# Optimization experiments

Measured on AMD Instinct MI355X. Metric: run time of the kernel, lower is better.

## Reference

```python
import jax, jax.numpy as jnp
import numpy as np

MARGIN = 0.3
NUM_CLASSES = 1000


def setup_inputs() -> dict:
    key = jax.random.key(0)
    k1, k2 = jax.random.split(key)
    B, D = 8192, 256
    inputs = jax.random.normal(k1, (B, D), dtype=jnp.float32)
    targets = jax.random.randint(k2, (B,), 0, NUM_CLASSES, dtype=jnp.int64)
    return {"inputs": inputs, "targets": targets}


def reference(inputs, targets):
    # Squared Euclidean pairwise distances: ||x_i||^2 + ||x_j||^2 - 2 x_i.x_j
    sq = jnp.sum(inputs * inputs, axis=1)                      # [B]
    dist = sq[:, None] + sq[None, :] - 2.0 * (inputs @ inputs.T)  # [B, B]

    # Hard mining: per-row max over positives (same label, incl. self),
    # min over negatives, exactly as the torch per-row masked max/min loop.
    pos_mask = targets[:, None] == targets[None, :]            # [B, B] bool
    neg_inf = jnp.float32(-jnp.inf)
    pos_inf = jnp.float32(jnp.inf)
    dist_ap = jnp.max(jnp.where(pos_mask, dist, neg_inf), axis=1)  # [B]
    dist_an = jnp.min(jnp.where(pos_mask, pos_inf, dist), axis=1)  # [B]

    # MarginRankingLoss(margin)(dist_an, dist_ap, y=1) = mean relu(ap - an + m)
    loss = jnp.mean(jax.nn.relu(dist_ap - dist_an + MARGIN))
    prec = jnp.mean((dist_an > dist_ap).astype(jnp.float32))
    return (loss, prec)
```

## Files before the change

kernel.cpp:

```cpp
#include <hip/hip_runtime.h>
#include <hip/hip_bf16.h>

#define B_N 8192
#define D_K 256
#define MARGIN 0.3f

typedef float f32x4 __attribute__((ext_vector_type(4)));
typedef short s16x8 __attribute__((ext_vector_type(8)));

__device__ __forceinline__ unsigned fkey(float f) {
    unsigned u = __float_as_uint(f);
    return (u & 0x80000000u) ? ~u : (u | 0x80000000u);
}
__device__ __forceinline__ float kval(unsigned k) {
    return (k & 0x80000000u) ? __uint_as_float(k ^ 0x80000000u)
                             : __uint_as_float(~k);
}

__device__ __forceinline__ void load_lds16(const unsigned short* g,
                                           unsigned short* l) {
    __builtin_amdgcn_global_load_lds(
        (const __attribute__((address_space(1))) unsigned int*)g,
        (__attribute__((address_space(3))) unsigned int*)l, 16, 0, 0);
}

__global__ __launch_bounds__(256) void prep_kernel(const float* __restrict__ X,
        float* __restrict__ sq, unsigned* __restrict__ apk,
        unsigned* __restrict__ ank, unsigned short* __restrict__ Xp,
        float* __restrict__ acc2) {
    int row  = (blockIdx.x << 2) + (threadIdx.x >> 6);
    int lane = threadIdx.x & 63;
    const float4 v = reinterpret_cast<const float4*>(X + (size_t)row * D_K)[lane];

    float xs[4] = {v.x, v.y, v.z, v.w};
    ushort4 hv;
    unsigned short* hp = &hv.x;
    float s = 0.f;
    #pragma unroll
    for (int i = 0; i < 4; ++i) {
        __hip_bfloat16 h = __float2bfloat16(xs[i]);
        hp[i] = *reinterpret_cast<unsigned short*>(&h);
        float hf = __bfloat162float(h);
        s = fmaf(hf, hf, s);
    }
    *reinterpret_cast<ushort4*>(Xp + (size_t)row * D_K + lane * 4) = hv;

    #pragma unroll
    for (int o = 32; o > 0; o >>= 1) s += __shfl_down(s, o, 64);
    if (lane == 0) {
        sq[row]  = s;
        apk[row] = 0u;
        ank[row] = 0xFFFFFFFFu;
    }
    if (blockIdx.x == 0 && threadIdx.x == 0) {
        acc2[0] = 0.f; acc2[1] = 0.f;
        reinterpret_cast<unsigned*>(acc2)[2] = 0u;
    }
}

#define BM 128
#define BN 128

__global__ __launch_bounds__(256, 4) void dist_kernel(
        const unsigned short* __restrict__ Xp,
        const int* __restrict__ tgt, const float* __restrict__ sq,
        unsigned* __restrict__ apk, unsigned* __restrict__ ank) {
    __shared__ unsigned short Atile[128 * 64];
    __shared__ unsigned short Btile[128 * 64];

    const int t    = threadIdx.x;
    const int lane = t & 63;
    const int wave = t >> 6;
    const int wrow = (wave >> 1) * 64;
    const int wcol = (wave & 1) * 64;
    const int fr   = lane & 15;
    const int quad = lane >> 4;
    const float INF = __int_as_float(0x7f800000);

    int tt = blockIdx.x;
    int bx = (int)((sqrtf(8.f * (float)tt + 1.f) - 1.f) * 0.5f);
    while ((bx + 1) * (bx + 2) / 2 <= tt) ++bx;
    while (bx * (bx + 1) / 2 > tt) --bx;
    int by = tt - bx * (bx + 1) / 2;
    const int bm = by * BM;
    const int bn = bx * BN;

    const unsigned short* ag[4];
    const unsigned short* bg[4];
    unsigned short* al[4];
    unsigned short* bl[4];
    #pragma unroll
    for (int j = 0; j < 4; ++j) {
        int g = wave * 64 + j * 256 + lane;
        int r = g >> 3, s0 = g & 7;
        int u = s0 ^ (r & 7);
        ag[j] = Xp + (size_t)(bm + r) * D_K + u * 8;
        bg[j] = Xp + (size_t)(bn + r) * D_K + u * 8;
        al[j] = Atile + g * 8;
        bl[j] = Btile + g * 8;
    }

    f32x4 acc[4][4];
    #pragma unroll
    for (int i = 0; i < 4; ++i)
        #pragma unroll
        for (int j = 0; j < 4; ++j) acc[i][j] = (f32x4){0.f, 0.f, 0.f, 0.f};

    #pragma unroll 1
    for (int win = 0; win < 4; ++win) {
        __syncthreads();
        const int wo = win * 64;
        #pragma unroll
        for (int j = 0; j < 4; ++j) {
            load_lds16(ag[j] + wo, al[j]);
            load_lds16(bg[j] + wo, bl[j]);
        }
        __syncthreads();

        s16x8 a[4][2], b[4][2];
        #pragma unroll
        for (int mi = 0; mi < 4; ++mi) {
            int rb = (wrow + mi * 16 + fr) * 64;
            #pragma unroll
            for (int h = 0; h < 2; ++h) {
                int s = (h * 4 + quad) ^ (fr & 7);
                a[mi][h] = *reinterpret_cast<const s16x8*>(&Atile[rb + s * 8]);
            }
        }
        #pragma unroll
        for (int ni = 0; ni < 4; ++ni) {
            int rb = (wcol + ni * 16 + fr) * 64;
            #pragma unroll
            for (int h = 0; h < 2; ++h) {
                int s = (h * 4 + quad) ^ (fr & 7);
                b[ni][h] = *reinterpret_cast<const s16x8*>(&Btile[rb + s * 8]);
            }
        }
        #pragma unroll
        for (int mi = 0; mi < 4; ++mi)
            #pragma unroll
            for (int ni = 0; ni < 4; ++ni) {
                acc[mi][ni] = __builtin_amdgcn_mfma_f32_16x16x32_bf16(
                    a[mi][0], b[ni][0], acc[mi][ni], 0, 0, 0);
                acc[mi][ni] = __builtin_amdgcn_mfma_f32_16x16x32_bf16(
                    a[mi][1], b[ni][1], acc[mi][ni], 0, 0, 0);
            }
    }

    int   ct[4]; float csq[4];
    #pragma unroll
    for (int ni = 0; ni < 4; ++ni) {
        int c = bn + wcol + ni * 16 + fr;
        ct[ni] = tgt[c]; csq[ni] = sq[c];
    }
    float cap[4], can[4];
    #pragma unroll
    for (int ni = 0; ni < 4; ++ni) { cap[ni] = -INF; can[ni] = INF; }

    #pragma unroll
    for (int mi = 0; mi < 4; ++mi) {
        #pragma unroll
        for (int reg = 0; reg < 4; ++reg) {
            int rl = wrow + mi * 16 + quad * 4 + reg;
            int rt = tgt[bm + rl]; float rsq = sq[bm + rl];
            float rap = -INF, ran = INF;
            #pragma unroll
            for (int ni = 0; ni < 4; ++ni) {
                float d = rsq + csq[ni] - 2.f * acc[mi][ni][reg];
                bool pos = (rt == ct[ni]);
                if (pos) { rap = fmaxf(rap, d); cap[ni] = fmaxf(cap[ni], d); }
                else     { ran = fminf(ran, d); can[ni] = fminf(can[ni], d); }
            }
            #pragma unroll
            for (int o = 1; o < 16; o <<= 1) {
                rap = fmaxf(rap, __shfl_xor(rap, o, 64));
                ran = fminf(ran, __shfl_xor(ran, o, 64));
            }
            if (fr == 0) {
                atomicMax(&apk[bm + rl], fkey(rap));
                atomicMin(&ank[bm + rl], fkey(ran));
            }
        }
    }
    #pragma unroll
    for (int ni = 0; ni < 4; ++ni) {
        #pragma unroll
        for (int o = 16; o < 64; o <<= 1) {
            cap[ni] = fmaxf(cap[ni], __shfl_xor(cap[ni], o, 64));
            can[ni] = fminf(can[ni], __shfl_xor(can[ni], o, 64));
        }
    }
    if (lane < 16) {
        #pragma unroll
        for (int ni = 0; ni < 4; ++ni) {
            int c = bn + wcol + ni * 16 + lane;
            atomicMax(&apk[c], fkey(cap[ni]));
            atomicMin(&ank[c], fkey(can[ni]));
        }
    }
}

__global__ __launch_bounds__(256) void final_kernel(const unsigned* __restrict__ apk,
        const unsigned* __restrict__ ank, float* __restrict__ acc2,
        float* __restrict__ out) {
    __shared__ float s_sum[4], s_cnt[4];
    int i = blockIdx.x * 256 + threadIdx.x;
    float ap = kval(apk[i]);
    float an = kval(ank[i]);
    float v  = ap - an + MARGIN;
    float sum = v > 0.f ? v : 0.f;
    float cnt = an > ap ? 1.f : 0.f;
    #pragma unroll
    for (int o = 32; o > 0; o >>= 1) {
        sum += __shfl_down(sum, o, 64);
        cnt += __shfl_down(cnt, o, 64);
    }
    int wave = threadIdx.x >> 6, lane = threadIdx.x & 63;
    if (lane == 0) { s_sum[wave] = sum; s_cnt[wave] = cnt; }
    __syncthreads();
    if (threadIdx.x == 0) {
        float ts = 0.f, tc = 0.f;
        #pragma unroll
        for (int w = 0; w < 4; ++w) { ts += s_sum[w]; tc += s_cnt[w]; }
        atomicAdd(&acc2[0], ts);
        atomicAdd(&acc2[1], tc);
        __threadfence();
        unsigned ticket = atomicAdd(reinterpret_cast<unsigned*>(acc2) + 2, 1u);
        if (ticket == gridDim.x - 1) {
            float fs = atomicAdd(&acc2[0], 0.f);
            float fc = atomicAdd(&acc2[1], 0.f);
            out[0] = fs / (float)B_N;
            out[1] = fc / (float)B_N;
        }
    }
}

extern "C" void kernel_launch(void* const* d_in, const int* in_sizes, int n_in,
                              void* d_out, int out_size, void* d_ws, size_t ws_size,
                              hipStream_t stream) {
    const float* X   = (const float*)d_in[0];
    const int*   tgt = (const int*)d_in[1];

    char* ws = (char*)d_ws;
    float*          sq   = (float*)ws;
    unsigned*       apk  = (unsigned*)(ws + 32768);
    unsigned*       ank  = (unsigned*)(ws + 65536);
    float*          acc2 = (float*)(ws + 98304);
    unsigned short* Xp   = (unsigned short*)(ws + 131072);

    float* out = (float*)d_out;

    prep_kernel<<<B_N / 4, 256, 0, stream>>>(X, sq, apk, ank, Xp, acc2);
    dist_kernel<<<(64 * 65) / 2, 256, 0, stream>>>(Xp, tgt, sq, apk, ank);
    final_kernel<<<B_N / 256, 256, 0, stream>>>(apk, ank, acc2, out);
}
```

Baseline: 118.3 us.

## Double-buffer LDS tiles in dist_kernel and hoist label/norm loads before the K loop

Doubles the A/B LDS tiles so the async global-to-LDS load of the next K window is issued while MFMAs run on the current one. This removes one barrier per iteration and hides the load latency. The row/column target and squared-norm loads are hoisted ahead of the main loop and LDS read offsets are precomputed. MFMA sections are wrapped in s_setprio. The doubled LDS footprint comes with a lower launch-bounds occupancy hint (4 to 2), which may reduce latency hiding across blocks.

```diff
diff --git a/kernel.cpp b/kernel.cpp
--- a/kernel.cpp
+++ b/kernel.cpp
@@ -61,12 +61,12 @@
 #define BM 128
 #define BN 128
 
-__global__ __launch_bounds__(256, 4) void dist_kernel(
+__global__ __launch_bounds__(256, 2) void dist_kernel(
         const unsigned short* __restrict__ Xp,
         const int* __restrict__ tgt, const float* __restrict__ sq,
         unsigned* __restrict__ apk, unsigned* __restrict__ ank) {
-    __shared__ unsigned short Atile[128 * 64];
-    __shared__ unsigned short Btile[128 * 64];
+    __shared__ unsigned short Atile[2][128 * 64];
+    __shared__ unsigned short Btile[2][128 * 64];
 
     const int t    = threadIdx.x;
     const int lane = t & 63;
@@ -85,10 +85,25 @@
     const int bm = by * BM;
     const int bn = bx * BN;
 
+    int ct[4]; float csq[4];
+    #pragma unroll
+    for (int ni = 0; ni < 4; ++ni) {
+        int c = bn + wcol + ni * 16 + fr;
+        ct[ni] = tgt[c]; csq[ni] = sq[c];
+    }
+    int rt[16]; float rsq[16];
+    #pragma unroll
+    for (int mi = 0; mi < 4; ++mi)
+        #pragma unroll
+        for (int reg = 0; reg < 4; ++reg) {
+            int r = bm + wrow + mi * 16 + quad * 4 + reg;
+            rt[mi * 4 + reg]  = tgt[r];
+            rsq[mi * 4 + reg] = sq[r];
+        }
+
     const unsigned short* ag[4];
     const unsigned short* bg[4];
-    unsigned short* al[4];
-    unsigned short* bl[4];
+    int loff[4];
     #pragma unroll
     for (int j = 0; j < 4; ++j) {
         int g = wave * 64 + j * 256 + lane;
@@ -96,8 +111,23 @@
         int u = s0 ^ (r & 7);
         ag[j] = Xp + (size_t)(bm + r) * D_K + u * 8;
         bg[j] = Xp + (size_t)(bn + r) * D_K + u * 8;
-        al[j] = Atile + g * 8;
-        bl[j] = Btile + g * 8;
+        loff[j] = g * 8;
+    }
+
+    int aoff[4][2], boff[4][2];
+    #pragma unroll
+    for (int mi = 0; mi < 4; ++mi)
+        #pragma unroll
+        for (int h = 0; h < 2; ++h) {
+            int s = (h * 4 + quad) ^ (fr & 7);
+            aoff[mi][h] = (wrow + mi * 16 + fr) * 64 + s * 8;
+            boff[mi][h] = (wcol + mi * 16 + fr) * 64 + s * 8;
+        }
+
+    #pragma unroll
+    for (int j = 0; j < 4; ++j) {
+        load_lds16(ag[j], &Atile[0][loff[j]]);
+        load_lds16(bg[j], &Btile[0][loff[j]]);
     }
 
     f32x4 acc[4][4];
@@ -106,36 +136,28 @@
         #pragma unroll
         for (int j = 0; j < 4; ++j) acc[i][j] = (f32x4){0.f, 0.f, 0.f, 0.f};
 
-    #pragma unroll 1
+    __syncthreads();
+
+    #pragma unroll
     for (int win = 0; win < 4; ++win) {
-        __syncthreads();
-        const int wo = win * 64;
-        #pragma unroll
-        for (int j = 0; j < 4; ++j) {
-            load_lds16(ag[j] + wo, al[j]);
-            load_lds16(bg[j] + wo, bl[j]);
-        }
-        __syncthreads();
-
+        const int cur = win & 1;
+        if (win < 3) {
+            const int wo = (win + 1) * 64;
+            #pragma unroll
+            for (int j = 0; j < 4; ++j) {
+                load_lds16(ag[j] + wo, &Atile[cur ^ 1][loff[j]]);
+                load_lds16(bg[j] + wo, &Btile[cur ^ 1][loff[j]]);
+            }
+        }
         s16x8 a[4][2], b[4][2];
         #pragma unroll
-        for (int mi = 0; mi < 4; ++mi) {
-            int rb = (wrow + mi * 16 + fr) * 64;
+        for (int mi = 0; mi < 4; ++mi)
             #pragma unroll
             for (int h = 0; h < 2; ++h) {
-                int s = (h * 4 + quad) ^ (fr & 7);
-                a[mi][h] = *reinterpret_cast<const s16x8*>(&Atile[rb + s * 8]);
-            }
-        }
-        #pragma unroll
-        for (int ni = 0; ni < 4; ++ni) {
-            int rb = (wcol + ni * 16 + fr) * 64;
-            #pragma unroll
-            for (int h = 0; h < 2; ++h) {
-                int s = (h * 4 + quad) ^ (fr & 7);
-                b[ni][h] = *reinterpret_cast<const s16x8*>(&Btile[rb + s * 8]);
-            }
-        }
+                a[mi][h] = *reinterpret_cast<const s16x8*>(&Atile[cur][aoff[mi][h]]);
+                b[mi][h] = *reinterpret_cast<const s16x8*>(&Btile[cur][boff[mi][h]]);
+            }
+        __builtin_amdgcn_s_setprio(1);
         #pragma unroll
         for (int mi = 0; mi < 4; ++mi)
             #pragma unroll
@@ -145,14 +167,10 @@
                 acc[mi][ni] = __builtin_amdgcn_mfma_f32_16x16x32_bf16(
                     a[mi][1], b[ni][1], acc[mi][ni], 0, 0, 0);
             }
-    }
-
-    int   ct[4]; float csq[4];
-    #pragma unroll
-    for (int ni = 0; ni < 4; ++ni) {
-        int c = bn + wcol + ni * 16 + fr;
-        ct[ni] = tgt[c]; csq[ni] = sq[c];
-    }
+        __builtin_amdgcn_s_setprio(0);
+        if (win < 3) __syncthreads();
+    }
+
     float cap[4], can[4];
     #pragma unroll
     for (int ni = 0; ni < 4; ++ni) { cap[ni] = -INF; can[ni] = INF; }
@@ -162,12 +180,13 @@
         #pragma unroll
         for (int reg = 0; reg < 4; ++reg) {
             int rl = wrow + mi * 16 + quad * 4 + reg;
-            int rt = tgt[bm + rl]; float rsq = sq[bm + rl];
+            int   rti  = rt[mi * 4 + reg];
+            float rsqi = rsq[mi * 4 + reg];
             float rap = -INF, ran = INF;
             #pragma unroll
             for (int ni = 0; ni < 4; ++ni) {
-                float d = rsq + csq[ni] - 2.f * acc[mi][ni][reg];
-                bool pos = (rt == ct[ni]);
+                float d = rsqi + csq[ni] - 2.f * acc[mi][ni][reg];
+                bool pos = (rti == ct[ni]);
                 if (pos) { rap = fmaxf(rap, d); cap[ni] = fmaxf(cap[ni], d); }
                 else     { ran = fminf(ran, d); can[ni] = fminf(can[ni], d); }
             }
```

After: 126.6 us. 1.07x slower.

## Load MFMA operands directly from global memory, dropping LDS staging and barriers

Applied to the files above, without the earlier changes.

The LDS tiles, async global-to-LDS loads and block barriers in the distance kernel are removed. Each wave now reads its A and B MFMA fragments straight from global memory (L2/L1 cached) with 16-byte vector loads, and the K loop is fully unrolled. This removes the barrier synchronisation and LDS traffic but loses operand sharing across waves, so each operand row is fetched from cache by two waves and the global access pattern becomes strided per lane.

```diff
diff --git a/kernel.cpp b/kernel.cpp
--- a/kernel.cpp
+++ b/kernel.cpp
@@ -15,13 +15,6 @@
 __device__ __forceinline__ float kval(unsigned k) {
     return (k & 0x80000000u) ? __uint_as_float(k ^ 0x80000000u)
                              : __uint_as_float(~k);
-}
-
-__device__ __forceinline__ void load_lds16(const unsigned short* g,
-                                           unsigned short* l) {
-    __builtin_amdgcn_global_load_lds(
-        (const __attribute__((address_space(1))) unsigned int*)g,
-        (__attribute__((address_space(3))) unsigned int*)l, 16, 0, 0);
 }
 
 __global__ __launch_bounds__(256) void prep_kernel(const float* __restrict__ X,
@@ -65,9 +58,6 @@
         const unsigned short* __restrict__ Xp,
         const int* __restrict__ tgt, const float* __restrict__ sq,
         unsigned* __restrict__ apk, unsigned* __restrict__ ank) {
-    __shared__ unsigned short Atile[128 * 64];
-    __shared__ unsigned short Btile[128 * 64];
-
     const int t    = threadIdx.x;
     const int lane = t & 63;
     const int wave = t >> 6;
@@ -85,20 +75,8 @@
     const int bm = by * BM;
     const int bn = bx * BN;
 
-    const unsigned short* ag[4];
-    const unsigned short* bg[4];
-    unsigned short* al[4];
-    unsigned short* bl[4];
-    #pragma unroll
-    for (int j = 0; j < 4; ++j) {
-        int g = wave * 64 + j * 256 + lane;
-        int r = g >> 3, s0 = g & 7;
-        int u = s0 ^ (r & 7);
-        ag[j] = Xp + (size_t)(bm + r) * D_K + u * 8;
-        bg[j] = Xp + (size_t)(bn + r) * D_K + u * 8;
-        al[j] = Atile + g * 8;
-        bl[j] = Btile + g * 8;
-    }
+    const unsigned short* abase = Xp + (size_t)(bm + wrow + fr) * D_K + quad * 8;
+    const unsigned short* bbase = Xp + (size_t)(bn + wcol + fr) * D_K + quad * 8;
 
     f32x4 acc[4][4];
     #pragma unroll
@@ -106,45 +84,28 @@
         #pragma unroll
         for (int j = 0; j < 4; ++j) acc[i][j] = (f32x4){0.f, 0.f, 0.f, 0.f};
 
-    #pragma unroll 1
+    #pragma unroll
     for (int win = 0; win < 4; ++win) {
-        __syncthreads();
-        const int wo = win * 64;
-        #pragma unroll
-        for (int j = 0; j < 4; ++j) {
-            load_lds16(ag[j] + wo, al[j]);
-            load_lds16(bg[j] + wo, bl[j]);
-        }
-        __syncthreads();
-
-        s16x8 a[4][2], b[4][2];
+        const unsigned short* aw = abase + win * 64;
+        const unsigned short* bw = bbase + win * 64;
+        s16x8 a[4][2];
         #pragma unroll
         for (int mi = 0; mi < 4; ++mi) {
-            int rb = (wrow + mi * 16 + fr) * 64;
+            a[mi][0] = *reinterpret_cast<const s16x8*>(aw + mi * 16 * D_K);
+            a[mi][1] = *reinterpret_cast<const s16x8*>(aw + mi * 16 * D_K + 32);
+        }
+        #pragma unroll
+        for (int ni = 0; ni < 4; ++ni) {
+            s16x8 b0 = *reinterpret_cast<const s16x8*>(bw + ni * 16 * D_K);
+            s16x8 b1 = *reinterpret_cast<const s16x8*>(bw + ni * 16 * D_K + 32);
             #pragma unroll
-            for (int h = 0; h < 2; ++h) {
-                int s = (h * 4 + quad) ^ (fr & 7);
-                a[mi][h] = *reinterpret_cast<const s16x8*>(&Atile[rb + s * 8]);
-            }
-        }
-        #pragma unroll
-        for (int ni = 0; ni < 4; ++ni) {
-            int rb = (wcol + ni * 16 + fr) * 64;
-            #pragma unroll
-            for (int h = 0; h < 2; ++h) {
-                int s = (h * 4 + quad) ^ (fr & 7);
-                b[ni][h] = *reinterpret_cast<const s16x8*>(&Btile[rb + s * 8]);
-            }
-        }
-        #pragma unroll
-        for (int mi = 0; mi < 4; ++mi)
-            #pragma unroll
-            for (int ni = 0; ni < 4; ++ni) {
+            for (int mi = 0; mi < 4; ++mi) {
                 acc[mi][ni] = __builtin_amdgcn_mfma_f32_16x16x32_bf16(
-                    a[mi][0], b[ni][0], acc[mi][ni], 0, 0, 0);
+                    a[mi][0], b0, acc[mi][ni], 0, 0, 0);
                 acc[mi][ni] = __builtin_amdgcn_mfma_f32_16x16x32_bf16(
-                    a[mi][1], b[ni][1], acc[mi][ni], 0, 0, 0);
-            }
+                    a[mi][1], b1, acc[mi][ni], 0, 0, 0);
+            }
+        }
     }
 
     int   ct[4]; float csq[4];
@@ -162,12 +123,13 @@
         #pragma unroll
         for (int reg = 0; reg < 4; ++reg) {
             int rl = wrow + mi * 16 + quad * 4 + reg;
-            int rt = tgt[bm + rl]; float rsq = sq[bm + rl];
+            int rti = tgt[bm + rl];
+            float rsqi = sq[bm + rl];
             float rap = -INF, ran = INF;
             #pragma unroll
             for (int ni = 0; ni < 4; ++ni) {
-                float d = rsq + csq[ni] - 2.f * acc[mi][ni][reg];
-                bool pos = (rt == ct[ni]);
+                float d = rsqi + csq[ni] - 2.f * acc[mi][ni][reg];
+                bool pos = (rti == ct[ni]);
                 if (pos) { rap = fmaxf(rap, d); cap[ni] = fmaxf(cap[ni], d); }
                 else     { ran = fminf(ran, d); can[ni] = fminf(can[ni], d); }
             }
```

Measured after the change: 163.9 us. 1.39x slower.

## Fuse final reduction into dist kernel and stage row reductions through LDS

Applied to the files above, without the earlier changes.

Row max/min partials are written to shared memory and reduced per row by one thread, replacing 16-lane shuffle trees and per-quad atomics. This cuts global atomic traffic on the row side. The final loss/precision kernel is removed: the last tile block, found with a ticket counter, reads all keys and writes the outputs, saving a kernel launch. The cost is a serial tail on one block, extra LDS use that may lower occupancy, and more barriers.

```diff
diff --git a/kernel.cpp b/kernel.cpp
--- a/kernel.cpp
+++ b/kernel.cpp
@@ -4,6 +4,7 @@
 #define B_N 8192
 #define D_K 256
 #define MARGIN 0.3f
+#define NTILE 2080
 
 typedef float f32x4 __attribute__((ext_vector_type(4)));
 typedef short s16x8 __attribute__((ext_vector_type(8)));
@@ -53,7 +54,6 @@
         ank[row] = 0xFFFFFFFFu;
     }
     if (blockIdx.x == 0 && threadIdx.x == 0) {
-        acc2[0] = 0.f; acc2[1] = 0.f;
         reinterpret_cast<unsigned*>(acc2)[2] = 0u;
     }
 }
@@ -64,9 +64,12 @@
 __global__ __launch_bounds__(256, 4) void dist_kernel(
         const unsigned short* __restrict__ Xp,
         const int* __restrict__ tgt, const float* __restrict__ sq,
-        unsigned* __restrict__ apk, unsigned* __restrict__ ank) {
-    __shared__ unsigned short Atile[128 * 64];
-    __shared__ unsigned short Btile[128 * 64];
+        unsigned* __restrict__ apk, unsigned* __restrict__ ank,
+        unsigned* __restrict__ tick, float* __restrict__ out) {
+    __shared__ __align__(16) float smem_f[2 * 128 * 33];
+    __shared__ unsigned lastflag;
+    unsigned short* Atile = reinterpret_cast<unsigned short*>(smem_f);
+    unsigned short* Btile = Atile + 128 * 64;
 
     const int t    = threadIdx.x;
     const int lane = t & 63;
@@ -147,6 +150,8 @@
             }
     }
 
+    __syncthreads();
+
     int   ct[4]; float csq[4];
     #pragma unroll
     for (int ni = 0; ni < 4; ++ni) {
@@ -157,6 +162,7 @@
     #pragma unroll
     for (int ni = 0; ni < 4; ++ni) { cap[ni] = -INF; can[ni] = INF; }
 
+    const int mcol = (wave & 1) * 16 + fr;
     #pragma unroll
     for (int mi = 0; mi < 4; ++mi) {
         #pragma unroll
@@ -171,17 +177,11 @@
                 if (pos) { rap = fmaxf(rap, d); cap[ni] = fmaxf(cap[ni], d); }
                 else     { ran = fminf(ran, d); can[ni] = fminf(can[ni], d); }
             }
-            #pragma unroll
-            for (int o = 1; o < 16; o <<= 1) {
-                rap = fmaxf(rap, __shfl_xor(rap, o, 64));
-                ran = fminf(ran, __shfl_xor(ran, o, 64));
-            }
-            if (fr == 0) {
-                atomicMax(&apk[bm + rl], fkey(rap));
-                atomicMin(&ank[bm + rl], fkey(ran));
-            }
-        }
-    }
+            smem_f[rl * 33 + mcol]        = rap;
+            smem_f[4224 + rl * 33 + mcol] = ran;
+        }
+    }
+
     #pragma unroll
     for (int ni = 0; ni < 4; ++ni) {
         #pragma unroll
@@ -198,39 +198,51 @@
             atomicMin(&ank[c], fkey(can[ni]));
         }
     }
-}
-
-__global__ __launch_bounds__(256) void final_kernel(const unsigned* __restrict__ apk,
-        const unsigned* __restrict__ ank, float* __restrict__ acc2,
-        float* __restrict__ out) {
-    __shared__ float s_sum[4], s_cnt[4];
-    int i = blockIdx.x * 256 + threadIdx.x;
-    float ap = kval(apk[i]);
-    float an = kval(ank[i]);
-    float v  = ap - an + MARGIN;
-    float sum = v > 0.f ? v : 0.f;
-    float cnt = an > ap ? 1.f : 0.f;
-    #pragma unroll
-    for (int o = 32; o > 0; o >>= 1) {
-        sum += __shfl_down(sum, o, 64);
-        cnt += __shfl_down(cnt, o, 64);
-    }
-    int wave = threadIdx.x >> 6, lane = threadIdx.x & 63;
-    if (lane == 0) { s_sum[wave] = sum; s_cnt[wave] = cnt; }
-    __syncthreads();
-    if (threadIdx.x == 0) {
-        float ts = 0.f, tc = 0.f;
-        #pragma unroll
-        for (int w = 0; w < 4; ++w) { ts += s_sum[w]; tc += s_cnt[w]; }
-        atomicAdd(&acc2[0], ts);
-        atomicAdd(&acc2[1], tc);
+
+    __syncthreads();
+    {
+        int arr = t >> 7;
+        int row = t & 127;
+        const float* p = smem_f + arr * 4224 + row * 33;
+        float v = p[0];
+        if (arr == 0) {
+            #pragma unroll
+            for (int j = 1; j < 32; ++j) v = fmaxf(v, p[j]);
+            atomicMax(&apk[bm + row], fkey(v));
+        } else {
+            #pragma unroll
+            for (int j = 1; j < 32; ++j) v = fminf(v, p[j]);
+            atomicMin(&ank[bm + row], fkey(v));
+        }
+    }
+
+    __threadfence();
+    __syncthreads();
+    if (t == 0) lastflag = (atomicAdd(tick, 1u) == NTILE - 1u) ? 1u : 0u;
+    __syncthreads();
+    if (lastflag) {
         __threadfence();
-        unsigned ticket = atomicAdd(reinterpret_cast<unsigned*>(acc2) + 2, 1u);
-        if (ticket == gridDim.x - 1) {
-            float fs = atomicAdd(&acc2[0], 0.f);
-            float fc = atomicAdd(&acc2[1], 0.f);
-            out[0] = fs / (float)B_N;
-            out[1] = fc / (float)B_N;
+        float sum = 0.f, cnt = 0.f;
+        for (int i = t; i < B_N; i += 256) {
+            float ap = kval(atomicOr(&apk[i], 0u));
+            float an = kval(atomicOr(&ank[i], 0u));
+            float v  = ap - an + MARGIN;
+            sum += v > 0.f ? v : 0.f;
+            cnt += an > ap ? 1.f : 0.f;
+        }
+        #pragma unroll
+        for (int o = 32; o > 0; o >>= 1) {
+            sum += __shfl_down(sum, o, 64);
+            cnt += __shfl_down(cnt, o, 64);
+        }
+        if (lane == 0) { smem_f[wave] = sum; smem_f[8 + wave] = cnt; }
+        __syncthreads();
+        if (t == 0) {
+            float ts = 0.f, tc = 0.f;
+            #pragma unroll
+            for (int w = 0; w < 4; ++w) { ts += smem_f[w]; tc += smem_f[8 + w]; }
+            out[0] = ts / (float)B_N;
+            out[1] = tc / (float)B_N;
         }
     }
 }
@@ -248,9 +260,9 @@
     float*          acc2 = (float*)(ws + 98304);
     unsigned short* Xp   = (unsigned short*)(ws + 131072);
 
+    unsigned* tick = reinterpret_cast<unsigned*>(acc2) + 2;
     float* out = (float*)d_out;
 
     prep_kernel<<<B_N / 4, 256, 0, stream>>>(X, sq, apk, ank, Xp, acc2);
-    dist_kernel<<<(64 * 65) / 2, 256, 0, stream>>>(Xp, tgt, sq, apk, ank);
-    final_kernel<<<B_N / 256, 256, 0, stream>>>(apk, ank, acc2, out);
-}
+    dist_kernel<<<NTILE, 256, 0, stream>>>(Xp, tgt, sq, apk, ank, tick, out);
+}
```

Measured after the change: 238.4 us. 102% more time.
